# Performance work log

Hardware: AMD Instinct MI355X
Metric: run time of the kernel (lower is better)

The kernel has to match this reference:

```python
import jax, jax.numpy as jnp
import numpy as np

N_ITER = 50  # default n_iter in entmax_bisect


def _entmax_bisect(X, alpha):
    """alpha-entmax via bisection (Peters et al.), over last axis.
    X: [..., d]; alpha: broadcastable to X[..., :1], values in (1, 2].
    """
    am1 = alpha - 1.0
    inv = 1.0 / am1
    Xs = X * am1
    d = X.shape[-1]
    max_val = jnp.max(Xs, axis=-1, keepdims=True)
    tau_lo = max_val - 1.0                      # max - gp(1, alpha)
    tau_hi = max_val - (1.0 / d) ** am1          # max - gp(1/d, alpha)  [note: gp(x)=x**(1/am1); (1/d)**(1/(1/am1))? see below]
    # gp(x, alpha) = x ** (1 / (alpha - 1)); so gp(1/d) = (1/d) ** inv
    tau_hi = max_val - (1.0 / d) ** inv
    f_lo = jnp.sum(jnp.clip(Xs - tau_lo, 0.0, None) ** inv, axis=-1, keepdims=True) - 1.0
    dm0 = tau_hi - tau_lo

    def step(carry, _):
        tau_lo, dm, _tau_m = carry
        dm = dm * 0.5
        tau_m = tau_lo + dm
        p_m = jnp.clip(Xs - tau_m, 0.0, None) ** inv
        f_m = jnp.sum(p_m, axis=-1, keepdims=True) - 1.0
        tau_lo = jnp.where(f_m * f_lo >= 0.0, tau_m, tau_lo)
        return (tau_lo, dm, tau_m), None

    (tau_lo, dm, tau_m), _ = jax.lax.scan(step, (tau_lo, dm0, tau_lo), None, length=N_ITER)
    p = jnp.clip(Xs - tau_m, 0.0, None) ** inv
    # ensure_sum_one=True
    return p / jnp.sum(p, axis=-1, keepdims=True)


def setup_inputs() -> dict:
    key = jax.random.key(0)
    k1, k2 = jax.random.split(key)
    B, H, Q, K = 4, 16, 1024, 1024
    att_scores = jax.random.normal(k1, (B, H, Q, K), dtype=jnp.float32)
    alpha = jax.random.uniform(k2, (H,), dtype=jnp.float32)  # raw in (0,1); mapped to (1.01, 1.99) inside reference
    return {"att_scores": att_scores, "alpha": alpha}


def reference(att_scores, alpha):
    # torch module: per-head alpha in [1.01, 2] (clamp(1+sigmoid(pre_alpha))).
    a = (1.01 + 0.98 * alpha).reshape(1, -1, 1, 1)  # [1, H, 1, 1], broadcasts over B, Q, K
    return _entmax_bisect(att_scores, a)
```

## Files before the change

### kernel.cpp

```cpp
#include <hip/hip_runtime.h>


__device__ __forceinline__ float wave_sum(float v) {
#pragma unroll
  for (int off = 32; off > 0; off >>= 1) v += __shfl_xor(v, off, 64);
  return v;
}
__device__ __forceinline__ float wave_max(float v) {
#pragma unroll
  for (int off = 32; off > 0; off >>= 1) v = fmaxf(v, __shfl_xor(v, off, 64));
  return v;
}

#define MAXIT 12

__global__ __launch_bounds__(256) void entmax_secant(
    const float* __restrict__ X, const float* __restrict__ A,
    float* __restrict__ O, int nrows) {
  __shared__ float          cval[4][1024];
  __shared__ unsigned short cidx[4][1024];

  const int lane = threadIdx.x & 63;
  const int wid  = threadIdx.x >> 6;
  const long long row = (long long)blockIdx.x * 4 + wid;
  if (row >= nrows) return;

  const float* xr = X + row * 1024;
  float* orow     = O + row * 1024;

  const int h = (int)((row >> 10) & 15);
  const float a   = 1.01f + 0.98f * A[h];
  const float am1 = a - 1.0f;
  const float inv = 1.0f / am1;

  float xs[16];
#pragma unroll
  for (int c = 0; c < 4; ++c) {
    float4 t = reinterpret_cast<const float4*>(xr)[c * 64 + lane];
    xs[4*c+0] = t.x * am1; xs[4*c+1] = t.y * am1;
    xs[4*c+2] = t.z * am1; xs[4*c+3] = t.w * am1;
  }
  float m = xs[0];
#pragma unroll
  for (int j = 1; j < 16; ++j) m = fmaxf(m, xs[j]);
  m = wave_max(m);
#pragma unroll
  for (int j = 0; j < 16; ++j) xs[j] -= m;

  int base = 0;
#pragma unroll
  for (int c = 0; c < 4; ++c) {
#pragma unroll
    for (int k = 0; k < 4; ++k) {
      const int j = 4*c + k;
      const bool act = xs[j] > -1.0f;
      const unsigned long long mk = __ballot(act);
      if (act) {
        const int pos = base + __popcll(mk & ((1ull << lane) - 1ull));
        cval[wid][pos] = xs[j];
        cidx[wid][pos] = (unsigned short)(c * 256 + lane * 4 + k);
      }
      base += __popcll(mk);
    }
  }
  const int nact   = __builtin_amdgcn_readfirstlane(base);
  const bool direct = (nact == 1024);
  int K;
  float vals[16];
  if (direct) {
    K = 16;
#pragma unroll
    for (int k = 0; k < 16; ++k) vals[k] = xs[k];
  } else {
    K = (nact + 63) >> 6;
    for (int pos = nact + lane; pos < (K << 6); pos += 64)
      cval[wid][pos] = -2.0f;
    asm volatile("s_waitcnt lgkmcnt(0)" ::: "memory");
#pragma unroll
    for (int k = 0; k < 16; ++k)
      if (k < K) vals[k] = cval[wid][lane + (k << 6)];
  }

  float lwlo = -10.0f * am1;
  float lwhi = 0.0f;
  float w = 1.0f, lw = 0.0f;
  float lw_p = 0.0f, lf_p = 0.0f;
  float p[16];
  float f = 1.0f;

  for (int it = 0; it < MAXIT; ++it) {
    float fs = 0.0f;
#pragma unroll
    for (int k = 0; k < 16; ++k)
      if (k < K) {
        float u  = fmaxf(vals[k] + w, 0.0f);
        float pe = __builtin_amdgcn_exp2f(
            inv * __builtin_amdgcn_logf(u));
        p[k] = pe; fs += pe;
      }
    f = wave_sum(fs);

    float lwnew;
    if (f > 0.0f) {
      if (fabsf(f - 1.0f) <= 1e-6f) break;
      const float lf = __builtin_amdgcn_logf(f);
      if (f > 1.0f) lwhi = lw; else lwlo = lw;
      const float si = (it == 0) ? am1 : (lw - lw_p) / (lf - lf_p);
      lw_p = lw; lf_p = lf;
      lwnew = lw - lf * si;
      if (!(si > 0.0f) || !(lwnew > lwlo) || !(lwnew < lwhi))
        lwnew = 0.5f * (lwlo + lwhi);
    } else {
      lwlo = lw;
      lwnew = 0.5f * (lwlo + lwhi);
    }
    const float wnew  = __builtin_amdgcn_exp2f(lwnew);
    const float delta = fabsf(wnew - w);
    if (!(delta > 8e-6f * fmaxf(fabsf(m - w), 1.0f))) break;
    w = wnew; lw = lwnew;
  }

  const float r = 1.0f / f;
  if (direct) {
#pragma unroll
    for (int c = 0; c < 4; ++c) {
      float4 t;
      t.x = p[4*c+0] * r; t.y = p[4*c+1] * r;
      t.z = p[4*c+2] * r; t.w = p[4*c+3] * r;
      reinterpret_cast<float4*>(orow)[c * 64 + lane] = t;
    }
  } else {
    const float4 z = make_float4(0.0f, 0.0f, 0.0f, 0.0f);
#pragma unroll
    for (int c = 0; c < 4; ++c)
      reinterpret_cast<float4*>(&cval[wid][0])[c * 64 + lane] = z;
    asm volatile("s_waitcnt lgkmcnt(0)" ::: "memory");
#pragma unroll
    for (int k = 0; k < 16; ++k)
      if (k < K) {
        const int pos = lane + (k << 6);
        if (pos < nact) cval[wid][cidx[wid][pos]] = p[k] * r;
      }
    asm volatile("s_waitcnt lgkmcnt(0)" ::: "memory");
#pragma unroll
    for (int c = 0; c < 4; ++c) {
      float4 t = reinterpret_cast<const float4*>(&cval[wid][0])[c * 64 + lane];
      reinterpret_cast<float4*>(orow)[c * 64 + lane] = t;
    }
  }
}

extern "C" void kernel_launch(void* const* d_in, const int* in_sizes, int n_in,
                              void* d_out, int out_size, void* d_ws, size_t ws_size,
                              hipStream_t stream) {
  const float* X = (const float*)d_in[0];
  const float* A = (const float*)d_in[1];
  float* O       = (float*)d_out;
  const int nrows = in_sizes[0] / 1024;
  const int blocks = (nrows + 3) / 4;
  hipLaunchKernelGGL(entmax_secant, dim3(blocks), dim3(256), 0, stream,
                     X, A, O, nrows);
}
```

Before: 111.9 us.

## Use DPP wave reductions, count-first compaction, and Newton first step for root finding

Swaps the shuffle-based wave reductions for DPP row operations followed by a readlane. Active elements are now counted with ballots before any compaction, so the LDS compaction is skipped when every element is active. The first solver iteration also computes the derivative sum, which allows a Newton step in place of a fixed-slope secant step and is meant to cut the iteration count. The trade-off is an extra reduction and multiply in the first pass, more complex bracket handling, and a change to the convergence path.

```diff
diff --git a/kernel.cpp b/kernel.cpp
--- a/kernel.cpp
+++ b/kernel.cpp
@@ -1,20 +1,43 @@
 #include <hip/hip_runtime.h>
 
 
-__device__ __forceinline__ float wave_sum(float v) {
-#pragma unroll
-  for (int off = 32; off > 0; off >>= 1) v += __shfl_xor(v, off, 64);
-  return v;
-}
-__device__ __forceinline__ float wave_max(float v) {
-#pragma unroll
-  for (int off = 32; off > 0; off >>= 1) v = fmaxf(v, __shfl_xor(v, off, 64));
-  return v;
+template <int CTRL, int RM>
+__device__ __forceinline__ float dpp_add(float x) {
+  int s = __builtin_amdgcn_update_dpp(0, __builtin_bit_cast(int, x),
+                                      CTRL, RM, 0xF, false);
+  return x + __builtin_bit_cast(float, s);
+}
+template <int CTRL, int RM>
+__device__ __forceinline__ float dpp_max(float x) {
+  int s = __builtin_amdgcn_update_dpp((int)0xFF800000,
+                                      __builtin_bit_cast(int, x),
+                                      CTRL, RM, 0xF, false);
+  return fmaxf(x, __builtin_bit_cast(float, s));
+}
+__device__ __forceinline__ float wave_sum(float x) {
+  x = dpp_add<0xB1, 0xF>(x);
+  x = dpp_add<0x4E, 0xF>(x);
+  x = dpp_add<0x141, 0xF>(x);
+  x = dpp_add<0x140, 0xF>(x);
+  x = dpp_add<0x142, 0xA>(x);
+  x = dpp_add<0x143, 0xC>(x);
+  return __builtin_bit_cast(float,
+      __builtin_amdgcn_readlane(__builtin_bit_cast(int, x), 63));
+}
+__device__ __forceinline__ float wave_max(float x) {
+  x = dpp_max<0xB1, 0xF>(x);
+  x = dpp_max<0x4E, 0xF>(x);
+  x = dpp_max<0x141, 0xF>(x);
+  x = dpp_max<0x140, 0xF>(x);
+  x = dpp_max<0x142, 0xA>(x);
+  x = dpp_max<0x143, 0xC>(x);
+  return __builtin_bit_cast(float,
+      __builtin_amdgcn_readlane(__builtin_bit_cast(int, x), 63));
 }
 
 #define MAXIT 12
 
-__global__ __launch_bounds__(256) void entmax_secant(
+__global__ __launch_bounds__(256) void entmax_dpp(
     const float* __restrict__ X, const float* __restrict__ A,
     float* __restrict__ O, int nrows) {
   __shared__ float          cval[4][1024];
@@ -32,6 +55,7 @@
   const float a   = 1.01f + 0.98f * A[h];
   const float am1 = a - 1.0f;
   const float inv = 1.0f / am1;
+  const float c1  = inv - 1.0f;
 
   float xs[16];
 #pragma unroll
@@ -47,32 +71,34 @@
 #pragma unroll
   for (int j = 0; j < 16; ++j) xs[j] -= m;
 
-  int base = 0;
-#pragma unroll
-  for (int c = 0; c < 4; ++c) {
-#pragma unroll
-    for (int k = 0; k < 4; ++k) {
-      const int j = 4*c + k;
-      const bool act = xs[j] > -1.0f;
-      const unsigned long long mk = __ballot(act);
-      if (act) {
-        const int pos = base + __popcll(mk & ((1ull << lane) - 1ull));
-        cval[wid][pos] = xs[j];
-        cidx[wid][pos] = (unsigned short)(c * 256 + lane * 4 + k);
-      }
-      base += __popcll(mk);
-    }
-  }
-  const int nact   = __builtin_amdgcn_readfirstlane(base);
-  const bool direct = (nact == 1024);
-  int K;
+  int nact = 0;
+#pragma unroll
+  for (int j = 0; j < 16; ++j)
+    nact += (int)__popcll(__ballot(xs[j] > -1.0f));
+  const int  K      = (nact + 63) >> 6;
+  const bool direct = (K == 16);
+
   float vals[16];
   if (direct) {
-    K = 16;
 #pragma unroll
     for (int k = 0; k < 16; ++k) vals[k] = xs[k];
   } else {
-    K = (nact + 63) >> 6;
+    int base = 0;
+#pragma unroll
+    for (int c = 0; c < 4; ++c) {
+#pragma unroll
+      for (int k = 0; k < 4; ++k) {
+        const int j = 4*c + k;
+        const bool act = xs[j] > -1.0f;
+        const unsigned long long mk = __ballot(act);
+        if (act) {
+          const int pos = base + __popcll(mk & ((1ull << lane) - 1ull));
+          cval[wid][pos] = xs[j];
+          cidx[wid][pos] = (unsigned short)(c * 256 + lane * 4 + k);
+        }
+        base += __popcll(mk);
+      }
+    }
     for (int pos = nact + lane; pos < (K << 6); pos += 64)
       cval[wid][pos] = -2.0f;
     asm volatile("s_waitcnt lgkmcnt(0)" ::: "memory");
@@ -84,40 +110,60 @@
   float lwlo = -10.0f * am1;
   float lwhi = 0.0f;
   float w = 1.0f, lw = 0.0f;
-  float lw_p = 0.0f, lf_p = 0.0f;
   float p[16];
-  float f = 1.0f;
-
-  for (int it = 0; it < MAXIT; ++it) {
-    float fs = 0.0f;
+  float f, lw_p, lf_p;
+  {
+    float fs = 0.0f, gs = 0.0f;
 #pragma unroll
     for (int k = 0; k < 16; ++k)
       if (k < K) {
-        float u  = fmaxf(vals[k] + w, 0.0f);
-        float pe = __builtin_amdgcn_exp2f(
-            inv * __builtin_amdgcn_logf(u));
-        p[k] = pe; fs += pe;
+        float u  = fmaxf(vals[k] + 1.0f, 0.0f);
+        float e  = __builtin_amdgcn_exp2f(c1 * __builtin_amdgcn_logf(u));
+        float pe = e * u;
+        p[k] = pe; fs += pe; gs += e;
       }
     f = wave_sum(fs);
-
-    float lwnew;
-    if (f > 0.0f) {
-      if (fabsf(f - 1.0f) <= 1e-6f) break;
-      const float lf = __builtin_amdgcn_logf(f);
-      if (f > 1.0f) lwhi = lw; else lwlo = lw;
-      const float si = (it == 0) ? am1 : (lw - lw_p) / (lf - lf_p);
-      lw_p = lw; lf_p = lf;
-      lwnew = lw - lf * si;
-      if (!(si > 0.0f) || !(lwnew > lwlo) || !(lwnew < lwhi))
-        lwnew = 0.5f * (lwlo + lwhi);
-    } else {
-      lwlo = lw;
-      lwnew = 0.5f * (lwlo + lwhi);
-    }
-    const float wnew  = __builtin_amdgcn_exp2f(lwnew);
-    const float delta = fabsf(wnew - w);
-    if (!(delta > 8e-6f * fmaxf(fabsf(m - w), 1.0f))) break;
-    w = wnew; lw = lwnew;
+    const float g = wave_sum(gs);
+    lw_p = 0.0f; lf_p = __builtin_amdgcn_logf(f);
+    if (fabsf(f - 1.0f) > 1e-6f) {
+      float lwn = -lf_p * f * am1 / g;
+      if (!(lwn > lwlo) || !(lwn < lwhi)) lwn = 0.5f * (lwlo + lwhi);
+      lwhi = 0.0f;  lwlo = fmaxf(lwlo, -10.0f * am1);
+      lwhi = fminf(lwhi, lw);
+      w = __builtin_amdgcn_exp2f(lwn); lw = lwn;
+
+      for (int it = 1; it < MAXIT; ++it) {
+        float fs2 = 0.0f;
+#pragma unroll
+        for (int k = 0; k < 16; ++k)
+          if (k < K) {
+            float u  = fmaxf(vals[k] + w, 0.0f);
+            float pe = __builtin_amdgcn_exp2f(
+                inv * __builtin_amdgcn_logf(u));
+            p[k] = pe; fs2 += pe;
+          }
+        f = wave_sum(fs2);
+
+        float lwnew;
+        if (f > 0.0f) {
+          if (fabsf(f - 1.0f) <= 1e-6f) break;
+          const float lf = __builtin_amdgcn_logf(f);
+          if (f > 1.0f) lwhi = lw; else lwlo = lw;
+          const float si = (lw - lw_p) / (lf - lf_p);
+          lw_p = lw; lf_p = lf;
+          lwnew = lw - lf * si;
+          if (!(si > 0.0f) || !(lwnew > lwlo) || !(lwnew < lwhi))
+            lwnew = 0.5f * (lwlo + lwhi);
+        } else {
+          lwlo = lw;
+          lwnew = 0.5f * (lwlo + lwhi);
+        }
+        const float wnew  = __builtin_amdgcn_exp2f(lwnew);
+        const float delta = fabsf(wnew - w);
+        if (!(delta > 8e-6f * fmaxf(fabsf(m - w), 1.0f))) break;
+        w = wnew; lw = lwnew;
+      }
+    }
   }
 
   const float r = 1.0f / f;
@@ -158,6 +204,6 @@
   float* O       = (float*)d_out;
   const int nrows = in_sizes[0] / 1024;
   const int blocks = (nrows + 3) / 4;
-  hipLaunchKernelGGL(entmax_secant, dim3(blocks), dim3(256), 0, stream,
+  hipLaunchKernelGGL(entmax_dpp, dim3(blocks), dim3(256), 0, stream,
                      X, A, O, nrows);
 }
```

New measurement: 99.16 us. 11.4% less time.
